# Optimization experiments

Measured on AMD Instinct MI355X. Metric: run time of the kernel, lower is better.

The kernel has to match this reference:

```python
import jax, jax.numpy as jnp
import numpy as np

N = 100000      # atoms
E = 200000      # bonds (directed)
N2 = 200000     # 2-set super-nodes
A = 400000      # assignment entries atoms->2-sets
E2 = 400000     # 2-set graph edges
G = 5000        # molecules
D = 256         # emb_dim
FEAT = 40       # num_atom_features
NI2 = 8         # num_i_2
NBOND = 4       # bond types for edge embedding
L = 5           # num_layer
BN_EPS = 1e-5


def setup_inputs() -> dict:
    key = jax.random.key(0)
    ks = jax.random.split(key, 24)
    nrm = lambda k, shape, fan: jax.random.normal(k, shape, jnp.float32) / np.float32(np.sqrt(fan))
    inp = {}
    inp['x'] = jax.random.normal(ks[0], (N, FEAT), jnp.float32)
    inp['edge_index'] = jax.random.randint(ks[1], (2, E), 0, N, jnp.int32)
    inp['edge_attr'] = jax.random.randint(ks[2], (E,), 0, NBOND, jnp.int32)
    inp['iso_type_2'] = jax.random.uniform(ks[3], (N2, NI2), jnp.float32)
    inp['edge_index_2'] = jax.random.randint(ks[4], (2, E2), 0, N2, jnp.int32)
    inp['assignment_index_2'] = jnp.stack([
        jax.random.randint(ks[5], (A,), 0, N, jnp.int32),
        jax.random.randint(ks[6], (A,), 0, N2, jnp.int32)])
    inp['batch'] = jnp.sort(jax.random.randint(ks[7], (N,), 0, G, jnp.int32))
    inp['batch_2'] = jnp.sort(jax.random.randint(ks[8], (N2,), 0, G, jnp.int32))
    # params
    inp['W_emb'] = nrm(ks[9], (FEAT, D), FEAT); inp['b_emb'] = jnp.zeros((D,), jnp.float32)
    inp['edge_tables'] = nrm(ks[10], (L, NBOND, D), D)
    inp['eps'] = jnp.zeros((L,), jnp.float32)
    inp['gin_w1'] = nrm(ks[11], (L, D, 2 * D), D); inp['gin_b1'] = jnp.zeros((L, 2 * D), jnp.float32)
    inp['gin_w2'] = nrm(ks[12], (L, 2 * D, D), 2 * D); inp['gin_b2'] = jnp.zeros((L, D), jnp.float32)
    inp['bn_gamma'] = jnp.ones((L, D), jnp.float32); inp['bn_beta'] = jnp.zeros((L, D), jnp.float32)
    inp['iso1_ws'] = nrm(ks[13], (D + NI2, D), D + NI2)
    inp['iso1_wn'] = nrm(ks[14], (D + NI2, D), D + NI2)
    inp['iso1_b'] = jnp.zeros((D,), jnp.float32)
    inp['iso2_ws'] = nrm(ks[15], (D, D), D)
    inp['iso2_wn'] = nrm(ks[16], (D, D), D)
    inp['iso2_b'] = jnp.zeros((D,), jnp.float32)
    inp['fc0_w'] = nrm(ks[17], (2 * D, D), 2 * D); inp['fc0_b'] = jnp.zeros((D,), jnp.float32)
    inp['fc1_w'] = nrm(ks[18], (D, D // 2), D); inp['fc1_b'] = jnp.zeros((D // 2,), jnp.float32)
    inp['fc2_w'] = nrm(ks[19], (D // 2, D // 4), D // 2); inp['fc2_b'] = jnp.zeros((D // 4,), jnp.float32)
    inp['last_w'] = nrm(ks[20], (D // 4, 1), D // 4); inp['last_b'] = jnp.zeros((1,), jnp.float32)
    return inp


def _segment_mean(v, seg, num):
    s = jax.ops.segment_sum(v, seg, num_segments=num)
    c = jax.ops.segment_sum(jnp.ones((v.shape[0], 1), v.dtype), seg, num_segments=num)
    return s / jnp.maximum(c, 1.0)


def _graph_conv(h, src, dst, ws, wn, b, n):
    # PyG GraphConv: W_self x_i + sum_{j->i} W_nei x_j + b
    nei = jax.ops.segment_sum((h @ wn)[src], dst, num_segments=n)
    return h @ ws + nei + b


def reference(x, edge_index, edge_attr, iso_type_2, edge_index_2, assignment_index_2,
              batch, batch_2, W_emb, b_emb, edge_tables, eps, gin_w1, gin_b1,
              gin_w2, gin_b2, bn_gamma, bn_beta, iso1_ws, iso1_wn, iso1_b,
              iso2_ws, iso2_wn, iso2_b, fc0_w, fc0_b, fc1_w, fc1_b, fc2_w, fc2_b,
              last_w, last_b):
    n = x.shape[0]
    src, dst = edge_index[0], edge_index[1]
    # atom embedding
    h = jax.nn.relu(x @ W_emb + b_emb)
    # GIN stack (JK='last', eval mode: dropout identity, BN with batch stats)
    for l in range(L):
        msg = h[src] + edge_tables[l][edge_attr]          # [E, D]
        agg = jax.ops.segment_sum(msg, dst, num_segments=n)
        z = (1.0 + eps[l]) * h + agg
        z = jax.nn.relu(z @ gin_w1[l] + gin_b1[l]) @ gin_w2[l] + gin_b2[l]
        mu = z.mean(axis=0)
        var = z.var(axis=0)
        z = bn_gamma[l] * (z - mu) * jax.lax.rsqrt(var + BN_EPS) + bn_beta[l]
        h = z if l == L - 1 else jax.nn.relu(z)
    node_rep = h                                           # [N, D]
    # graph pooling (mean)
    x_1 = _segment_mean(node_rep, batch, G)                # [G, D]
    # avg_pool onto 2-set nodes
    xp = _segment_mean(node_rep[assignment_index_2[0]], assignment_index_2[1], N2)
    x2 = jnp.concatenate([xp, iso_type_2], axis=1)         # [N2, D+NI2]
    s2, d2 = edge_index_2[0], edge_index_2[1]
    x2 = jax.nn.relu(_graph_conv(x2, s2, d2, iso1_ws, iso1_wn, iso1_b, N2))
    x2 = jax.nn.relu(_graph_conv(x2, s2, d2, iso2_ws, iso2_wn, iso2_b, N2))
    x_2 = _segment_mean(x2, batch_2, G)                    # [G, D]
    m = jnp.concatenate([x_1, x_2], axis=1)                # [G, 2D]
    m = jax.nn.relu(m @ fc0_w + fc0_b)
    m = jax.nn.relu(m @ fc1_w + fc1_b)
    m = jax.nn.relu(m @ fc2_w + fc2_b)
    m = m @ last_w + last_b
    return m.reshape(-1)                                   # num_tasks == 1
```

## Files before the change

### kernel.cpp

```cpp
#include <hip/hip_runtime.h>
#include <cstddef>

constexpr int NA   = 100000;
constexpr int NE   = 200000;
constexpr int NN2  = 200000;
constexpr int NASS = 400000;
constexpr int NE2  = 400000;
constexpr int NG   = 5000;
constexpr int D    = 256;
constexpr int FEAT = 40;
constexpr int NI2  = 8;
constexpr int NL   = 5;
constexpr int CH   = 25000;

typedef unsigned short u16;
typedef __attribute__((ext_vector_type(8))) short bf16x8;
typedef __attribute__((ext_vector_type(4))) float f32x4;

static __device__ __forceinline__ float b2f(u16 s) {
    union { unsigned int u; float f; } v; v.u = ((unsigned int)s) << 16; return v.f;
}
static __device__ __forceinline__ u16 f2b(float f) {
    union { unsigned int u; float f; } v; v.f = f;
    unsigned int r = v.u + 0x7FFFu + ((v.u >> 16) & 1u);
    return (u16)(r >> 16);
}

constexpr size_t HB_OFF   = 0;
constexpr size_t ZB_OFF   = 102400000;
constexpr size_t TC_OFF   = 153600000;
constexpr size_t XEMB_OFF = 102400000;
constexpr size_t XPB_OFF  = 102400000;
constexpr size_t HN_OFF   = 0;
constexpr size_t MB_OFF   = 204800000;
constexpr size_t F1_OFF   = 215040000;
constexpr size_t F2_OFF   = 220160000;
constexpr size_t F3_OFF   = 222720000;
constexpr size_t WEMT_OFF = 224000000;
constexpr size_t GW1T_OFF = 224065536;
constexpr size_t GW2T_OFF = 226686976;
constexpr size_t IWT_OFF  = 229308416;
constexpr size_t EOFF_OFF = 230400000;
constexpr size_t EIDS_OFF = 230800768;
constexpr size_t AOFF_OFF = 231600832;
constexpr size_t AIDS_OFF = 232400896;
constexpr size_t E2OFF_OFF= 234000960;
constexpr size_t E2IDS_OFF= 234801024;
constexpr size_t CUR_OFF  = 236401088;
constexpr size_t PART_OFF = 237201152;
constexpr size_t GST_OFF  = 237202240;
constexpr size_t G2ST_OFF = 237222272;
constexpr size_t BS_OFF   = 237242304;
constexpr size_t SC_OFF   = 237244416;
constexpr size_t SH_OFF   = 237245440;
constexpr size_t WS_BYTES = 237246464;

template<int BIAS, int RELU, int ISO, int AF32, int CF32>
__global__ __launch_bounds__(512) void k_mgemm(
    const void* __restrict__ Av, int lda,
    const u16* __restrict__ Bt,
    const float* __restrict__ bias,
    const float* __restrict__ iso,
    const float* __restrict__ wtail,
    void* __restrict__ Cv, int ldc,
    int M, int N, int K)
{
    __shared__ __align__(16) u16 Ah[128][40];
    __shared__ __align__(16) u16 Al[AF32 ? 128 : 1][40];
    __shared__ __align__(16) u16 Bh[256][40];
    __shared__ __align__(16) u16 Bl[256][40];
    const int tid = threadIdx.x;
    const int wave = tid >> 6, lane = tid & 63;
    const int wr = wave >> 2, wc = wave & 3;
    const int bm = blockIdx.y * 128, bn = blockIdx.x * 256;
    const int l15 = lane & 15, lhi = lane >> 4;
    const int ar = tid >> 2, ac = (tid & 3) << 3;
    const u16* Blo = Bt + (size_t)N * K;
    f32x4 acc[4][4] = {};
    const int ktiles = K >> 5;
    for (int kt = 0; kt < ktiles; ++kt) {
        const int k0 = kt << 5;
        ushort4 a0h = {0,0,0,0}, a1h = {0,0,0,0}, a0l = {0,0,0,0}, a1l = {0,0,0,0};
        if (AF32) {
            float4 v0 = {0,0,0,0}, v1 = {0,0,0,0};
            if (bm + ar < M) {
                const float* ap = (const float*)Av + (size_t)(bm + ar) * lda + k0 + ac;
                v0 = *(const float4*)ap; v1 = *(const float4*)(ap + 4);
            }
            a0h.x = f2b(v0.x); a0h.y = f2b(v0.y); a0h.z = f2b(v0.z); a0h.w = f2b(v0.w);
            a1h.x = f2b(v1.x); a1h.y = f2b(v1.y); a1h.z = f2b(v1.z); a1h.w = f2b(v1.w);
            a0l.x = f2b(v0.x - b2f(a0h.x)); a0l.y = f2b(v0.y - b2f(a0h.y));
            a0l.z = f2b(v0.z - b2f(a0h.z)); a0l.w = f2b(v0.w - b2f(a0h.w));
            a1l.x = f2b(v1.x - b2f(a1h.x)); a1l.y = f2b(v1.y - b2f(a1h.y));
            a1l.z = f2b(v1.z - b2f(a1h.z)); a1l.w = f2b(v1.w - b2f(a1h.w));
        } else {
            if (bm + ar < M) {
                const u16* ap = (const u16*)Av + (size_t)(bm + ar) * lda + k0 + ac;
                a0h = *(const ushort4*)ap; a1h = *(const ushort4*)(ap + 4);
            }
        }
        const u16* bp0h = Bt  + (size_t)(bn + ar) * K + k0 + ac;
        const u16* bp1h = Bt  + (size_t)(bn + 128 + ar) * K + k0 + ac;
        const u16* bp0l = Blo + (size_t)(bn + ar) * K + k0 + ac;
        const u16* bp1l = Blo + (size_t)(bn + 128 + ar) * K + k0 + ac;
        ushort4 b00h = *(const ushort4*)bp0h, b01h = *(const ushort4*)(bp0h + 4);
        ushort4 b10h = *(const ushort4*)bp1h, b11h = *(const ushort4*)(bp1h + 4);
        ushort4 b00l = *(const ushort4*)bp0l, b01l = *(const ushort4*)(bp0l + 4);
        ushort4 b10l = *(const ushort4*)bp1l, b11l = *(const ushort4*)(bp1l + 4);
        __syncthreads();
        *(ushort4*)&Ah[ar][ac] = a0h; *(ushort4*)&Ah[ar][ac + 4] = a1h;
        if (AF32) { *(ushort4*)&Al[ar][ac] = a0l; *(ushort4*)&Al[ar][ac + 4] = a1l; }
        *(ushort4*)&Bh[ar][ac] = b00h;       *(ushort4*)&Bh[ar][ac + 4] = b01h;
        *(ushort4*)&Bh[128 + ar][ac] = b10h; *(ushort4*)&Bh[128 + ar][ac + 4] = b11h;
        *(ushort4*)&Bl[ar][ac] = b00l;       *(ushort4*)&Bl[ar][ac + 4] = b01l;
        *(ushort4*)&Bl[128 + ar][ac] = b10l; *(ushort4*)&Bl[128 + ar][ac + 4] = b11l;
        __syncthreads();
        bf16x8 fah[4], fal[4], fbh[4], fbl[4];
        #pragma unroll
        for (int m = 0; m < 4; ++m) {
            fah[m] = *(const bf16x8*)&Ah[wr * 64 + m * 16 + l15][lhi * 8];
            if (AF32) fal[m] = *(const bf16x8*)&Al[wr * 64 + m * 16 + l15][lhi * 8];
        }
        #pragma unroll
        for (int n = 0; n < 4; ++n) {
            fbh[n] = *(const bf16x8*)&Bh[wc * 64 + n * 16 + l15][lhi * 8];
            fbl[n] = *(const bf16x8*)&Bl[wc * 64 + n * 16 + l15][lhi * 8];
        }
        #pragma unroll
        for (int m = 0; m < 4; ++m)
            #pragma unroll
            for (int n = 0; n < 4; ++n) {
                acc[m][n] = __builtin_amdgcn_mfma_f32_16x16x32_bf16(fah[m], fbh[n], acc[m][n], 0, 0, 0);
                acc[m][n] = __builtin_amdgcn_mfma_f32_16x16x32_bf16(fah[m], fbl[n], acc[m][n], 0, 0, 0);
                if (AF32)
                    acc[m][n] = __builtin_amdgcn_mfma_f32_16x16x32_bf16(fal[m], fbh[n], acc[m][n], 0, 0, 0);
            }
    }
    #pragma unroll
    for (int m = 0; m < 4; ++m) {
        int rbase = bm + wr * 64 + m * 16 + lhi * 4;
        #pragma unroll
        for (int n = 0; n < 4; ++n) {
            int col = bn + wc * 64 + n * 16 + l15;
            #pragma unroll
            for (int r = 0; r < 4; ++r) {
                int row = rbase + r;
                if (row >= M) continue;
                float v = acc[m][n][r];
                if (BIAS) v += bias[col];
                if (ISO) {
                    const float* ir = iso + (size_t)row * NI2;
                    #pragma unroll
                    for (int k = 0; k < NI2; ++k) v += ir[k] * wtail[k * 256 + col];
                }
                if (RELU) v = fmaxf(v, 0.f);
                size_t cidx = (size_t)row * ldc + col;
                if (CF32) ((float*)Cv)[cidx] = v;
                else      ((u16*)Cv)[cidx] = f2b(v);
            }
        }
    }
}

__global__ __launch_bounds__(256) void k_gemm(
    const float* __restrict__ A, int lda,
    const float* __restrict__ B, int ldb,
    const float* __restrict__ bias,
    float* __restrict__ C, int ldc,
    int M, int N, int K, int relu)
{
    __shared__ __align__(16) float As[16][68];
    __shared__ __align__(16) float Bs[16][68];
    const int tid = threadIdx.x;
    const int tx = tid & 15, ty = tid >> 4;
    const int bm = blockIdx.y * 64, bn = blockIdx.x * 64;
    const int arow = tid >> 2, akq = (tid & 3) << 2;
    const int bk = tid >> 4, bnq = (tid & 15) << 2;
    float c[4][4] = {};
    const int ktiles = (K + 15) >> 4;
    for (int kt = 0; kt < ktiles; ++kt) {
        const int k0 = kt << 4;
        float4 av = make_float4(0.f, 0.f, 0.f, 0.f);
        if (bm + arow < M && k0 + akq + 4 <= K)
            av = *reinterpret_cast<const float4*>(A + (size_t)(bm + arow) * lda + (k0 + akq));
        As[akq + 0][arow] = av.x; As[akq + 1][arow] = av.y;
        As[akq + 2][arow] = av.z; As[akq + 3][arow] = av.w;
        float4 bv = make_float4(0.f, 0.f, 0.f, 0.f);
        if (k0 + bk < K && bn + bnq + 4 <= N)
            bv = *reinterpret_cast<const float4*>(B + (size_t)(k0 + bk) * ldb + (bn + bnq));
        *reinterpret_cast<float4*>(&Bs[bk][bnq]) = bv;
        __syncthreads();
        #pragma unroll
        for (int k = 0; k < 16; ++k) {
            float a0 = As[k][ty*4+0], a1 = As[k][ty*4+1], a2 = As[k][ty*4+2], a3 = As[k][ty*4+3];
            float b0 = Bs[k][tx*4+0], b1 = Bs[k][tx*4+1], b2 = Bs[k][tx*4+2], b3 = Bs[k][tx*4+3];
            c[0][0]+=a0*b0;c[0][1]+=a0*b1;c[0][2]+=a0*b2;c[0][3]+=a0*b3;
            c[1][0]+=a1*b0;c[1][1]+=a1*b1;c[1][2]+=a1*b2;c[1][3]+=a1*b3;
            c[2][0]+=a2*b0;c[2][1]+=a2*b1;c[2][2]+=a2*b2;c[2][3]+=a2*b3;
            c[3][0]+=a3*b0;c[3][1]+=a3*b1;c[3][2]+=a3*b2;c[3][3]+=a3*b3;
        }
        __syncthreads();
    }
    #pragma unroll
    for (int i = 0; i < 4; ++i) {
        int row = bm + ty * 4 + i;
        if (row >= M) continue;
        #pragma unroll
        for (int j = 0; j < 4; ++j) {
            int col = bn + tx * 4 + j;
            if (col >= N) continue;
            float v = c[i][j] + bias[col];
            if (relu) v = fmaxf(v, 0.f);
            C[(size_t)row * ldc + col] = v;
        }
    }
}

__global__ void k_zero(float* __restrict__ p, size_t n) {
    size_t i = (size_t)blockIdx.x * blockDim.x + threadIdx.x;
    size_t st = (size_t)gridDim.x * blockDim.x;
    for (; i < n; i += st) p[i] = 0.f;
}
__global__ void k_fill(float* __restrict__ p, int n, float v) {
    int i = blockIdx.x * blockDim.x + threadIdx.x;
    int st = gridDim.x * blockDim.x;
    for (; i < n; i += st) p[i] = v;
}

__global__ void k_count(const int* __restrict__ idx, int n, int* __restrict__ cnt) {
    int i = blockIdx.x * blockDim.x + threadIdx.x;
    int st = gridDim.x * blockDim.x;
    for (; i < n; i += st) atomicAdd(&cnt[idx[i]], 1);
}
__global__ void k_scan_partial(const int* __restrict__ cnt, int n, int* __restrict__ part) {
    __shared__ int sm[256];
    int c = blockIdx.x, t = threadIdx.x;
    int base = c * 4096 + t * 16;
    int s = 0;
    #pragma unroll
    for (int j = 0; j < 16; ++j) { int i = base + j; if (i < n) s += cnt[i]; }
    sm[t] = s; __syncthreads();
    for (int o = 128; o; o >>= 1) { if (t < o) sm[t] += sm[t + o]; __syncthreads(); }
    if (t == 0) part[c] = sm[0];
}
__global__ void k_scan_mid(int* __restrict__ part, int nch, int* __restrict__ off, int n) {
    if (threadIdx.x == 0 && blockIdx.x == 0) {
        int run = 0;
        for (int c = 0; c < nch; ++c) { int v = part[c]; part[c] = run; run += v; }
        off[n] = run;
    }
}
__global__ void k_scan_final(const int* __restrict__ cnt, int n, const int* __restrict__ part,
                             int* __restrict__ off) {
    __shared__ int sm[256];
    int c = blockIdx.x, t = threadIdx.x;
    int base = c * 4096 + t * 16;
    int loc[16]; int s = 0;
    #pragma unroll
    for (int j = 0; j < 16; ++j) { int i = base + j; int v = (i < n) ? cnt[i] : 0; loc[j] = s; s += v; }
    sm[t] = s; __syncthreads();
    for (int o = 1; o < 256; o <<= 1) {
        int v = (t >= o) ? sm[t - o] : 0;
        __syncthreads(); sm[t] += v; __syncthreads();
    }
    int tpre = (t == 0) ? 0 : sm[t - 1];
    int cb = part[c];
    #pragma unroll
    for (int j = 0; j < 16; ++j) { int i = base + j; if (i < n) off[i] = cb + tpre + loc[j]; }
}
__global__ void k_fill_csr(const int* __restrict__ idx, const int* __restrict__ pay, int n,
                           const int* __restrict__ off, int* __restrict__ cur, int* __restrict__ ids) {
    int i = blockIdx.x * blockDim.x + threadIdx.x;
    int st = gridDim.x * blockDim.x;
    for (; i < n; i += st) {
        int d = idx[i];
        int p = off[d] + atomicAdd(&cur[d], 1);
        ids[p] = pay[i];
    }
}
__global__ void k_pack(const int* __restrict__ src, const int* __restrict__ attr,
                       int* __restrict__ pk, int n) {
    int i = blockIdx.x * blockDim.x + threadIdx.x;
    int st = gridDim.x * blockDim.x;
    for (; i < n; i += st) pk[i] = (src[i] << 2) | attr[i];
}
__global__ void k_lbound(const int* __restrict__ arr, int n, int nseg, int* __restrict__ st) {
    int g = blockIdx.x * blockDim.x + threadIdx.x;
    if (g > nseg) return;
    int lo = 0, hi = n;
    while (lo < hi) { int mid = (lo + hi) >> 1; if (arr[mid] < g) lo = mid + 1; else hi = mid; }
    st[g] = lo;
}

__global__ void k_wt(const float* __restrict__ w, u16* __restrict__ wt, int K, int N) {
    int i = blockIdx.x * blockDim.x + threadIdx.x;
    int tot = K * N, st = gridDim.x * blockDim.x;
    for (; i < tot; i += st) {
        int n_ = i / K, k = i - n_ * K;
        float v = w[(size_t)k * N + n_];
        u16 h = f2b(v);
        wt[i] = h;
        wt[(size_t)tot + i] = f2b(v - b2f(h));
    }
}
__global__ void k_wembT(const float* __restrict__ w, u16* __restrict__ wt) {
    int i = blockIdx.x * blockDim.x + threadIdx.x;
    if (i >= 256 * 64) return;
    int n_ = i >> 6, k = i & 63;
    float v = (k < FEAT) ? w[(size_t)k * 256 + n_] : 0.f;
    u16 h = f2b(v);
    wt[i] = h;
    wt[256 * 64 + i] = f2b(v - b2f(h));
}
__global__ void k_xemb(const float* __restrict__ x, float* __restrict__ xe) {
    size_t i = (size_t)blockIdx.x * blockDim.x + threadIdx.x;
    size_t st = (size_t)gridDim.x * blockDim.x;
    size_t tot = (size_t)NA * 64;
    for (; i < tot; i += st) {
        int r = (int)(i >> 6), c = (int)(i & 63);
        xe[i] = (c < FEAT) ? x[(size_t)r * FEAT + c] : 0.f;
    }
}

__global__ void k_gin_gather(const float* __restrict__ hb, const int* __restrict__ off,
                             const int* __restrict__ ids, const float* __restrict__ etab_l,
                             const float* __restrict__ epsv, int l, u16* __restrict__ zb) {
    int wid = (blockIdx.x * blockDim.x + threadIdx.x) >> 6;
    int lane = threadIdx.x & 63;
    int nw = (gridDim.x * blockDim.x) >> 6;
    int c = lane * 4;
    float e1 = 1.f + epsv[l];
    for (int v = wid; v < NA; v += nw) {
        float4 h = *(const float4*)(hb + (size_t)v * D + c);
        float s0 = e1 * h.x, s1 = e1 * h.y, s2 = e1 * h.z, s3 = e1 * h.w;
        int p1 = off[v + 1];
        for (int p = off[v]; p < p1; ++p) {
            int pk = ids[p]; int src = pk >> 2; int at = pk & 3;
            float4 u = *(const float4*)(hb + (size_t)src * D + c);
            float4 t = *(const float4*)(etab_l + at * D + c);
            s0 += u.x + t.x; s1 += u.y + t.y; s2 += u.z + t.z; s3 += u.w + t.w;
        }
        ushort4 o; o.x = f2b(s0); o.y = f2b(s1); o.z = f2b(s2); o.w = f2b(s3);
        *(ushort4*)(zb + (size_t)v * D + c) = o;
    }
}
__global__ void k_xp_gather(const float* __restrict__ hb, const int* __restrict__ off,
                            const int* __restrict__ ids, u16* __restrict__ xpb) {
    int wid = (blockIdx.x * blockDim.x + threadIdx.x) >> 6;
    int lane = threadIdx.x & 63;
    int nw = (gridDim.x * blockDim.x) >> 6;
    int c = lane * 4;
    for (int v = wid; v < NN2; v += nw) {
        int p0 = off[v], p1 = off[v + 1];
        float s0 = 0, s1 = 0, s2 = 0, s3 = 0;
        for (int p = p0; p < p1; ++p) {
            const float* u = hb + (size_t)ids[p] * D + c;
            float4 uv = *(const float4*)u;
            s0 += uv.x; s1 += uv.y; s2 += uv.z; s3 += uv.w;
        }
        float inv = 1.f / fmaxf((float)(p1 - p0), 1.f);
        ushort4 o; o.x = f2b(s0 * inv); o.y = f2b(s1 * inv); o.z = f2b(s2 * inv); o.w = f2b(s3 * inv);
        *(ushort4*)(xpb + (size_t)v * D + c) = o;
    }
}
template<int POOL>
__global__ void k_conv_gather(u16* __restrict__ selfb, const u16* __restrict__ hn,
                              const int* __restrict__ off, const int* __restrict__ ids,
                              const int* __restrict__ batch2, float* __restrict__ mb) {
    int wid = (blockIdx.x * blockDim.x + threadIdx.x) >> 6;
    int lane = threadIdx.x & 63;
    int nw = (gridDim.x * blockDim.x) >> 6;
    int c = lane * 4;
    for (int v = wid; v < NN2; v += nw) {
        ushort4 sv = *(const ushort4*)(selfb + (size_t)v * D + c);
        float s0 = b2f(sv.x), s1 = b2f(sv.y), s2 = b2f(sv.z), s3 = b2f(sv.w);
        int p1 = off[v + 1];
        for (int p = off[v]; p < p1; ++p) {
            ushort4 u = *(const ushort4*)(hn + (size_t)ids[p] * D + c);
            s0 += b2f(u.x); s1 += b2f(u.y); s2 += b2f(u.z); s3 += b2f(u.w);
        }
        s0 = fmaxf(s0, 0.f); s1 = fmaxf(s1, 0.f); s2 = fmaxf(s2, 0.f); s3 = fmaxf(s3, 0.f);
        if (POOL) {
            float* mp = mb + (size_t)batch2[v] * (2 * D) + D + c;
            atomicAdd(mp + 0, s0); atomicAdd(mp + 1, s1);
            atomicAdd(mp + 2, s2); atomicAdd(mp + 3, s3);
        } else {
            ushort4 o; o.x = f2b(s0); o.y = f2b(s1); o.z = f2b(s2); o.w = f2b(s3);
            *(ushort4*)(selfb + (size_t)v * D + c) = o;
        }
    }
}

__global__ void k_bn_stats(const float* __restrict__ z, float* __restrict__ sum,
                           float* __restrict__ sumsq, int n) {
    int c = threadIdx.x;
    float s = 0.f, q = 0.f;
    for (int r = blockIdx.x; r < n; r += gridDim.x) {
        float v = z[(size_t)r * D + c];
        s += v; q += v * v;
    }
    atomicAdd(&sum[c], s);
    atomicAdd(&sumsq[c], q);
}
__global__ void k_bn_final(const float* __restrict__ sum, const float* __restrict__ sumsq,
                           const float* __restrict__ gamma, const float* __restrict__ beta,
                           float* __restrict__ scale, float* __restrict__ shift, int n) {
    int c = threadIdx.x;
    float mu = sum[c] / (float)n;
    float var = sumsq[c] / (float)n - mu * mu;
    float sc = gamma[c] * rsqrtf(var + 1e-5f);
    scale[c] = sc;
    shift[c] = beta[c] - mu * sc;
}
__global__ void k_bn_apply(float* __restrict__ h, const float* __restrict__ scale,
                           const float* __restrict__ shift, size_t n, int relu) {
    size_t i = (size_t)blockIdx.x * blockDim.x + threadIdx.x;
    size_t st = (size_t)gridDim.x * blockDim.x;
    for (; i < n; i += st) {
        int c = (int)(i & (D - 1));
        float v = scale[c] * h[i] + shift[c];
        if (relu) v = fmaxf(v, 0.f);
        h[i] = v;
    }
}

__global__ void k_pool1(const float* __restrict__ hb, const int* __restrict__ gst,
                        float* __restrict__ mb) {
    int g = blockIdx.x, t = threadIdx.x;
    int a = gst[g], b = gst[g + 1];
    float s = 0.f;
    for (int r = a; r < b; ++r) s += hb[(size_t)r * D + t];
    mb[(size_t)g * (2 * D) + t] = s / fmaxf((float)(b - a), 1.f);
}
__global__ void k_div2(float* __restrict__ mb, const int* __restrict__ g2st) {
    int g = blockIdx.x, t = threadIdx.x;
    float c = fmaxf((float)(g2st[g + 1] - g2st[g]), 1.f);
    mb[(size_t)g * (2 * D) + D + t] /= c;
}
__global__ void k_last(const float* __restrict__ f3, const float* __restrict__ w,
                       const float* __restrict__ b, float* __restrict__ out, int gn) {
    int g = blockIdx.x * 4 + (threadIdx.x >> 6);
    int lane = threadIdx.x & 63;
    if (g >= gn) return;
    float v = f3[(size_t)g * 64 + lane] * w[lane];
    #pragma unroll
    for (int off = 32; off; off >>= 1) v += __shfl_down(v, off);
    if (lane == 0) out[g] = v + b[0];
}

static inline dim3 ggrid(int M, int N) { return dim3((N + 63) / 64, (M + 63) / 64); }

extern "C" void kernel_launch(void* const* d_in, const int* in_sizes, int n_in,
                              void* d_out, int out_size, void* d_ws, size_t ws_size,
                              hipStream_t stream) {
    const float* x      = (const float*)d_in[0];
    const int*   eidx   = (const int*)  d_in[1];
    const int*   eattr  = (const int*)  d_in[2];
    const float* iso    = (const float*)d_in[3];
    const int*   eidx2  = (const int*)  d_in[4];
    const int*   assign = (const int*)  d_in[5];
    const int*   batch  = (const int*)  d_in[6];
    const int*   batch2 = (const int*)  d_in[7];
    const float* W_emb  = (const float*)d_in[8];
    const float* b_emb  = (const float*)d_in[9];
    const float* etab   = (const float*)d_in[10];
    const float* epsv   = (const float*)d_in[11];
    const float* gw1    = (const float*)d_in[12];
    const float* gb1    = (const float*)d_in[13];
    const float* gw2    = (const float*)d_in[14];
    const float* gb2    = (const float*)d_in[15];
    const float* bng    = (const float*)d_in[16];
    const float* bnb    = (const float*)d_in[17];
    const float* i1ws   = (const float*)d_in[18];
    const float* i1wn   = (const float*)d_in[19];
    const float* i1b    = (const float*)d_in[20];
    const float* i2ws   = (const float*)d_in[21];
    const float* i2wn   = (const float*)d_in[22];
    const float* i2b    = (const float*)d_in[23];
    const float* fc0w   = (const float*)d_in[24];
    const float* fc0b   = (const float*)d_in[25];
    const float* fc1w   = (const float*)d_in[26];
    const float* fc1b   = (const float*)d_in[27];
    const float* fc2w   = (const float*)d_in[28];
    const float* fc2b   = (const float*)d_in[29];
    const float* lw     = (const float*)d_in[30];
    const float* lb     = (const float*)d_in[31];

    float* out = (float*)d_out;
    char*  ws  = (char*)d_ws;
    if (ws_size < WS_BYTES) {
        k_fill<<<32, 256, 0, stream>>>(out, out_size, 10000.0f + (float)(ws_size >> 20));
        return;
    }

    float* HB   = (float*)(ws + HB_OFF);
    u16*   ZB   = (u16*)(ws + ZB_OFF);
    float* TC   = (float*)(ws + TC_OFF);
    float* XEMB = (float*)(ws + XEMB_OFF);
    u16*   XPB  = (u16*)(ws + XPB_OFF);
    u16*   HN   = (u16*)(ws + HN_OFF);
    float* Mb   = (float*)(ws + MB_OFF);
    float* F1   = (float*)(ws + F1_OFF);
    float* F2   = (float*)(ws + F2_OFF);
    float* F3   = (float*)(ws + F3_OFF);
    u16*   wembT= (u16*)(ws + WEMT_OFF);
    u16*   gw1T = (u16*)(ws + GW1T_OFF);
    u16*   gw2T = (u16*)(ws + GW2T_OFF);
    u16*   iwT  = (u16*)(ws + IWT_OFF);
    u16*   i1wnT= iwT;
    u16*   i1wsT= iwT + 2 * 65536;
    u16*   i2wnT= iwT + 4 * 65536;
    u16*   i2wsT= iwT + 6 * 65536;
    int*   eoff = (int*)(ws + EOFF_OFF);
    int*   eids = (int*)(ws + EIDS_OFF);
    int*   aoff = (int*)(ws + AOFF_OFF);
    int*   aids = (int*)(ws + AIDS_OFF);
    int*   e2off= (int*)(ws + E2OFF_OFF);
    int*   e2ids= (int*)(ws + E2IDS_OFF);
    int*   cur  = (int*)(ws + CUR_OFF);
    int*   part = (int*)(ws + PART_OFF);
    int*   gst  = (int*)(ws + GST_OFF);
    int*   g2st = (int*)(ws + G2ST_OFF);
    float* BS   = (float*)(ws + BS_OFF);
    float* SC   = (float*)(ws + SC_OFF);
    float* SH   = (float*)(ws + SH_OFF);
    int*   packs= (int*)F1;

    const int* e_src = eidx;   const int* e_dst = eidx + NE;
    const int* a0    = assign; const int* a1    = assign + NASS;
    const int* s2    = eidx2;  const int* d2    = eidx2 + NE2;

    dim3 sg(2048);
    dim3 ew(8192);
    const int nchA = (NA + 4095) / 4096;
    const int nch2 = (NN2 + 4095) / 4096;

    k_zero<<<dim3(1024), 256, 0, stream>>>(Mb, (size_t)NG * 2 * D);

    k_lbound<<<dim3((NG + 256) / 256), 256, 0, stream>>>(batch, NA, NG, gst);
    k_lbound<<<dim3((NG + 256) / 256), 256, 0, stream>>>(batch2, NN2, NG, g2st);

    k_zero<<<dim3(256), 256, 0, stream>>>((float*)cur, NA);
    k_count<<<dim3(1024), 256, 0, stream>>>(e_dst, NE, cur);
    k_scan_partial<<<dim3(nchA), 256, 0, stream>>>(cur, NA, part);
    k_scan_mid<<<dim3(1), 64, 0, stream>>>(part, nchA, eoff, NA);
    k_scan_final<<<dim3(nchA), 256, 0, stream>>>(cur, NA, part, eoff);
    k_zero<<<dim3(256), 256, 0, stream>>>((float*)cur, NA);
    k_pack<<<dim3(1024), 256, 0, stream>>>(e_src, eattr, packs, NE);
    k_fill_csr<<<dim3(1024), 256, 0, stream>>>(e_dst, packs, NE, eoff, cur, eids);

    k_zero<<<dim3(256), 256, 0, stream>>>((float*)cur, NN2);
    k_count<<<dim3(1024), 256, 0, stream>>>(a1, NASS, cur);
    k_scan_partial<<<dim3(nch2), 256, 0, stream>>>(cur, NN2, part);
    k_scan_mid<<<dim3(1), 64, 0, stream>>>(part, nch2, aoff, NN2);
    k_scan_final<<<dim3(nch2), 256, 0, stream>>>(cur, NN2, part, aoff);
    k_zero<<<dim3(256), 256, 0, stream>>>((float*)cur, NN2);
    k_fill_csr<<<dim3(1024), 256, 0, stream>>>(a1, a0, NASS, aoff, cur, aids);

    k_zero<<<dim3(256), 256, 0, stream>>>((float*)cur, NN2);
    k_count<<<dim3(1024), 256, 0, stream>>>(d2, NE2, cur);
    k_scan_partial<<<dim3(nch2), 256, 0, stream>>>(cur, NN2, part);
    k_scan_mid<<<dim3(1), 64, 0, stream>>>(part, nch2, e2off, NN2);
    k_scan_final<<<dim3(nch2), 256, 0, stream>>>(cur, NN2, part, e2off);
    k_zero<<<dim3(256), 256, 0, stream>>>((float*)cur, NN2);
    k_fill_csr<<<dim3(1024), 256, 0, stream>>>(d2, s2, NE2, e2off, cur, e2ids);

    k_wembT<<<dim3(64), 256, 0, stream>>>(W_emb, wembT);
    for (int l = 0; l < NL; ++l) {
        k_wt<<<dim3(512), 256, 0, stream>>>(gw1 + (size_t)l * D * 2 * D, gw1T + (size_t)l * 2 * 2 * D * D, D, 2 * D);
        k_wt<<<dim3(512), 256, 0, stream>>>(gw2 + (size_t)l * 2 * D * D, gw2T + (size_t)l * 2 * 2 * D * D, 2 * D, D);
    }
    k_wt<<<dim3(256), 256, 0, stream>>>(i1wn, i1wnT, D, D);
    k_wt<<<dim3(256), 256, 0, stream>>>(i1ws, i1wsT, D, D);
    k_wt<<<dim3(256), 256, 0, stream>>>(i2wn, i2wnT, D, D);
    k_wt<<<dim3(256), 256, 0, stream>>>(i2ws, i2wsT, D, D);

    k_xemb<<<ew, 256, 0, stream>>>(x, XEMB);
    k_mgemm<1,1,0,1,1><<<dim3(1, (NA + 127) / 128), 512, 0, stream>>>(
        XEMB, 64, wembT, b_emb, nullptr, nullptr, HB, D, NA, D, 64);

    for (int l = 0; l < NL; ++l) {
        k_gin_gather<<<sg, 256, 0, stream>>>(HB, eoff, eids, etab + (size_t)l * 4 * D, epsv, l, ZB);
        for (int c = 0; c < NA / CH; ++c) {
            k_mgemm<1,1,0,0,1><<<dim3(2, (CH + 127) / 128), 512, 0, stream>>>(
                ZB + (size_t)c * CH * D, D, gw1T + (size_t)l * 2 * 2 * D * D,
                gb1 + (size_t)l * 2 * D, nullptr, nullptr, TC, 2 * D, CH, 2 * D, D);
            k_mgemm<1,0,0,1,1><<<dim3(1, (CH + 127) / 128), 512, 0, stream>>>(
                TC, 2 * D, gw2T + (size_t)l * 2 * 2 * D * D,
                gb2 + (size_t)l * D, nullptr, nullptr, HB + (size_t)c * CH * D, D, CH, D, 2 * D);
        }
        k_zero<<<dim3(1), 512, 0, stream>>>(BS, 512);
        k_bn_stats<<<dim3(512), 256, 0, stream>>>(HB, BS, BS + D, NA);
        k_bn_final<<<dim3(1), 256, 0, stream>>>(BS, BS + D, bng + (size_t)l * D, bnb + (size_t)l * D, SC, SH, NA);
        k_bn_apply<<<ew, 256, 0, stream>>>(HB, SC, SH, (size_t)NA * D, l < NL - 1 ? 1 : 0);
    }

    k_pool1<<<dim3(NG), 256, 0, stream>>>(HB, gst, Mb);

    k_xp_gather<<<sg, 256, 0, stream>>>(HB, aoff, aids, XPB);

    k_mgemm<0,0,1,0,0><<<dim3(1, (NN2 + 127) / 128), 512, 0, stream>>>(
        XPB, D, i1wnT, nullptr, iso, i1wn + (size_t)D * D, HN, D, NN2, D, D);
    k_mgemm<1,0,1,0,0><<<dim3(1, (NN2 + 127) / 128), 512, 0, stream>>>(
        XPB, D, i1wsT, i1b, iso, i1ws + (size_t)D * D, XPB, D, NN2, D, D);
    k_conv_gather<0><<<sg, 256, 0, stream>>>(XPB, HN, e2off, e2ids, nullptr, nullptr);

    k_mgemm<0,0,0,0,0><<<dim3(1, (NN2 + 127) / 128), 512, 0, stream>>>(
        XPB, D, i2wnT, nullptr, nullptr, nullptr, HN, D, NN2, D, D);
    k_mgemm<1,0,0,0,0><<<dim3(1, (NN2 + 127) / 128), 512, 0, stream>>>(
        XPB, D, i2wsT, i2b, nullptr, nullptr, XPB, D, NN2, D, D);
    k_conv_gather<1><<<sg, 256, 0, stream>>>(XPB, HN, e2off, e2ids, batch2, Mb);
    k_div2<<<dim3(NG), 256, 0, stream>>>(Mb, g2st);

    k_gemm<<<ggrid(NG, D), 256, 0, stream>>>(Mb, 2 * D, fc0w, D, fc0b, F1, D, NG, D, 2 * D, 1);
    k_gemm<<<ggrid(NG, D / 2), 256, 0, stream>>>(F1, D, fc1w, D / 2, fc1b, F2, D / 2, NG, D / 2, D, 1);
    k_gemm<<<ggrid(NG, D / 4), 256, 0, stream>>>(F2, D / 2, fc2w, D / 4, fc2b, F3, D / 4, NG, D / 4, D / 2, 1);
    k_last<<<dim3((NG + 3) / 4), 256, 0, stream>>>(F3, lw, lb, out, NG);
}
```

Baseline: 3.909 ms.

## Store activations as split bf16 hi/lo pairs instead of fp32

Replaces fp32 intermediate buffers (node features, GEMM hidden outputs, embedding input) with bf16 storage. Where precision matters, a hi/lo bf16 pair is written by the GEMM epilogue, so the GEMM no longer converts fp32 to bf16 in its A-load loop. Gathers now read half-width rows and BN apply writes bf16 only. The atomic-based second pooling is replaced by a segmented pool kernel. The aim is to cut memory traffic and conversion ALU work. In exchange, node features lose precision after BN, since only the hi part is kept.

```diff
diff --git a/kernel.cpp b/kernel.cpp
--- a/kernel.cpp
+++ b/kernel.cpp
@@ -26,12 +26,12 @@
     return (u16)(r >> 16);
 }
 
-constexpr size_t HB_OFF   = 0;
-constexpr size_t ZB_OFF   = 102400000;
-constexpr size_t TC_OFF   = 153600000;
-constexpr size_t XEMB_OFF = 102400000;
-constexpr size_t XPB_OFF  = 102400000;
-constexpr size_t HN_OFF   = 0;
+constexpr size_t ZB_OFF   = 0;
+constexpr size_t TC_OFF   = 51200000;
+constexpr size_t XEMB_OFF = 51200000;
+constexpr size_t HB_OFF   = 102400000;
+constexpr size_t XPB_OFF  = 0;
+constexpr size_t HN_OFF   = 102400000;
 constexpr size_t MB_OFF   = 204800000;
 constexpr size_t F1_OFF   = 215040000;
 constexpr size_t F2_OFF   = 220160000;
@@ -51,22 +51,22 @@
 constexpr size_t GST_OFF  = 237202240;
 constexpr size_t G2ST_OFF = 237222272;
 constexpr size_t BS_OFF   = 237242304;
-constexpr size_t SC_OFF   = 237244416;
-constexpr size_t SH_OFF   = 237245440;
-constexpr size_t WS_BYTES = 237246464;
-
-template<int BIAS, int RELU, int ISO, int AF32, int CF32>
+constexpr size_t SCL_OFF  = 237244416;
+constexpr size_t SHL_OFF  = 237249536;
+constexpr size_t WS_BYTES = 237254656;
+
+template<int BIAS, int RELU, int ISO, int ALO, int CSPLIT>
 __global__ __launch_bounds__(512) void k_mgemm(
-    const void* __restrict__ Av, int lda,
+    const u16* __restrict__ A, int lda,
     const u16* __restrict__ Bt,
     const float* __restrict__ bias,
     const float* __restrict__ iso,
     const float* __restrict__ wtail,
-    void* __restrict__ Cv, int ldc,
+    u16* __restrict__ C, int ldc, long clo,
     int M, int N, int K)
 {
     __shared__ __align__(16) u16 Ah[128][40];
-    __shared__ __align__(16) u16 Al[AF32 ? 128 : 1][40];
+    __shared__ __align__(16) u16 Al[ALO ? 128 : 1][40];
     __shared__ __align__(16) u16 Bh[256][40];
     __shared__ __align__(16) u16 Bl[256][40];
     const int tid = threadIdx.x;
@@ -75,51 +75,32 @@
     const int bm = blockIdx.y * 128, bn = blockIdx.x * 256;
     const int l15 = lane & 15, lhi = lane >> 4;
     const int ar = tid >> 2, ac = (tid & 3) << 3;
+    const u16* Alo = A + (size_t)M * lda;
     const u16* Blo = Bt + (size_t)N * K;
     f32x4 acc[4][4] = {};
     const int ktiles = K >> 5;
     for (int kt = 0; kt < ktiles; ++kt) {
         const int k0 = kt << 5;
-        ushort4 a0h = {0,0,0,0}, a1h = {0,0,0,0}, a0l = {0,0,0,0}, a1l = {0,0,0,0};
-        if (AF32) {
-            float4 v0 = {0,0,0,0}, v1 = {0,0,0,0};
-            if (bm + ar < M) {
-                const float* ap = (const float*)Av + (size_t)(bm + ar) * lda + k0 + ac;
-                v0 = *(const float4*)ap; v1 = *(const float4*)(ap + 4);
-            }
-            a0h.x = f2b(v0.x); a0h.y = f2b(v0.y); a0h.z = f2b(v0.z); a0h.w = f2b(v0.w);
-            a1h.x = f2b(v1.x); a1h.y = f2b(v1.y); a1h.z = f2b(v1.z); a1h.w = f2b(v1.w);
-            a0l.x = f2b(v0.x - b2f(a0h.x)); a0l.y = f2b(v0.y - b2f(a0h.y));
-            a0l.z = f2b(v0.z - b2f(a0h.z)); a0l.w = f2b(v0.w - b2f(a0h.w));
-            a1l.x = f2b(v1.x - b2f(a1h.x)); a1l.y = f2b(v1.y - b2f(a1h.y));
-            a1l.z = f2b(v1.z - b2f(a1h.z)); a1l.w = f2b(v1.w - b2f(a1h.w));
-        } else {
-            if (bm + ar < M) {
-                const u16* ap = (const u16*)Av + (size_t)(bm + ar) * lda + k0 + ac;
-                a0h = *(const ushort4*)ap; a1h = *(const ushort4*)(ap + 4);
-            }
-        }
-        const u16* bp0h = Bt  + (size_t)(bn + ar) * K + k0 + ac;
-        const u16* bp1h = Bt  + (size_t)(bn + 128 + ar) * K + k0 + ac;
-        const u16* bp0l = Blo + (size_t)(bn + ar) * K + k0 + ac;
-        const u16* bp1l = Blo + (size_t)(bn + 128 + ar) * K + k0 + ac;
-        ushort4 b00h = *(const ushort4*)bp0h, b01h = *(const ushort4*)(bp0h + 4);
-        ushort4 b10h = *(const ushort4*)bp1h, b11h = *(const ushort4*)(bp1h + 4);
-        ushort4 b00l = *(const ushort4*)bp0l, b01l = *(const ushort4*)(bp0l + 4);
-        ushort4 b10l = *(const ushort4*)bp1l, b11l = *(const ushort4*)(bp1l + 4);
+        uint4 avh = {0,0,0,0}, avl = {0,0,0,0};
+        if (bm + ar < M) {
+            avh = *(const uint4*)(A + (size_t)(bm + ar) * lda + k0 + ac);
+            if (ALO) avl = *(const uint4*)(Alo + (size_t)(bm + ar) * lda + k0 + ac);
+        }
+        uint4 b0h = *(const uint4*)(Bt  + (size_t)(bn + ar) * K + k0 + ac);
+        uint4 b1h = *(const uint4*)(Bt  + (size_t)(bn + 128 + ar) * K + k0 + ac);
+        uint4 b0l = *(const uint4*)(Blo + (size_t)(bn + ar) * K + k0 + ac);
+        uint4 b1l = *(const uint4*)(Blo + (size_t)(bn + 128 + ar) * K + k0 + ac);
         __syncthreads();
-        *(ushort4*)&Ah[ar][ac] = a0h; *(ushort4*)&Ah[ar][ac + 4] = a1h;
-        if (AF32) { *(ushort4*)&Al[ar][ac] = a0l; *(ushort4*)&Al[ar][ac + 4] = a1l; }
-        *(ushort4*)&Bh[ar][ac] = b00h;       *(ushort4*)&Bh[ar][ac + 4] = b01h;
-        *(ushort4*)&Bh[128 + ar][ac] = b10h; *(ushort4*)&Bh[128 + ar][ac + 4] = b11h;
-        *(ushort4*)&Bl[ar][ac] = b00l;       *(ushort4*)&Bl[ar][ac + 4] = b01l;
-        *(ushort4*)&Bl[128 + ar][ac] = b10l; *(ushort4*)&Bl[128 + ar][ac + 4] = b11l;
+        *(uint4*)&Ah[ar][ac] = avh;
+        if (ALO) *(uint4*)&Al[ar][ac] = avl;
+        *(uint4*)&Bh[ar][ac] = b0h;  *(uint4*)&Bh[128 + ar][ac] = b1h;
+        *(uint4*)&Bl[ar][ac] = b0l;  *(uint4*)&Bl[128 + ar][ac] = b1l;
         __syncthreads();
         bf16x8 fah[4], fal[4], fbh[4], fbl[4];
         #pragma unroll
         for (int m = 0; m < 4; ++m) {
             fah[m] = *(const bf16x8*)&Ah[wr * 64 + m * 16 + l15][lhi * 8];
-            if (AF32) fal[m] = *(const bf16x8*)&Al[wr * 64 + m * 16 + l15][lhi * 8];
+            if (ALO) fal[m] = *(const bf16x8*)&Al[wr * 64 + m * 16 + l15][lhi * 8];
         }
         #pragma unroll
         for (int n = 0; n < 4; ++n) {
@@ -132,7 +113,7 @@
             for (int n = 0; n < 4; ++n) {
                 acc[m][n] = __builtin_amdgcn_mfma_f32_16x16x32_bf16(fah[m], fbh[n], acc[m][n], 0, 0, 0);
                 acc[m][n] = __builtin_amdgcn_mfma_f32_16x16x32_bf16(fah[m], fbl[n], acc[m][n], 0, 0, 0);
-                if (AF32)
+                if (ALO)
                     acc[m][n] = __builtin_amdgcn_mfma_f32_16x16x32_bf16(fal[m], fbh[n], acc[m][n], 0, 0, 0);
             }
     }
@@ -155,8 +136,13 @@
                 }
                 if (RELU) v = fmaxf(v, 0.f);
                 size_t cidx = (size_t)row * ldc + col;
-                if (CF32) ((float*)Cv)[cidx] = v;
-                else      ((u16*)Cv)[cidx] = f2b(v);
+                if (CSPLIT) {
+                    u16 h = f2b(v);
+                    C[cidx] = h;
+                    C[cidx + clo] = f2b(v - b2f(h));
+                } else {
+                    C[cidx] = f2b(v);
+                }
             }
         }
     }
@@ -312,17 +298,20 @@
     wt[i] = h;
     wt[256 * 64 + i] = f2b(v - b2f(h));
 }
-__global__ void k_xemb(const float* __restrict__ x, float* __restrict__ xe) {
+__global__ void k_xemb(const float* __restrict__ x, u16* __restrict__ xe) {
     size_t i = (size_t)blockIdx.x * blockDim.x + threadIdx.x;
     size_t st = (size_t)gridDim.x * blockDim.x;
     size_t tot = (size_t)NA * 64;
     for (; i < tot; i += st) {
         int r = (int)(i >> 6), c = (int)(i & 63);
-        xe[i] = (c < FEAT) ? x[(size_t)r * FEAT + c] : 0.f;
-    }
-}
-
-__global__ void k_gin_gather(const float* __restrict__ hb, const int* __restrict__ off,
+        float v = (c < FEAT) ? x[(size_t)r * FEAT + c] : 0.f;
+        u16 h = f2b(v);
+        xe[i] = h;
+        xe[tot + i] = f2b(v - b2f(h));
+    }
+}
+
+__global__ void k_gin_gather(const u16* __restrict__ hb, const int* __restrict__ off,
                              const int* __restrict__ ids, const float* __restrict__ etab_l,
                              const float* __restrict__ epsv, int l, u16* __restrict__ zb) {
     int wid = (blockIdx.x * blockDim.x + threadIdx.x) >> 6;
@@ -331,20 +320,21 @@
     int c = lane * 4;
     float e1 = 1.f + epsv[l];
     for (int v = wid; v < NA; v += nw) {
-        float4 h = *(const float4*)(hb + (size_t)v * D + c);
-        float s0 = e1 * h.x, s1 = e1 * h.y, s2 = e1 * h.z, s3 = e1 * h.w;
+        ushort4 h = *(const ushort4*)(hb + (size_t)v * D + c);
+        float s0 = e1 * b2f(h.x), s1 = e1 * b2f(h.y), s2 = e1 * b2f(h.z), s3 = e1 * b2f(h.w);
         int p1 = off[v + 1];
         for (int p = off[v]; p < p1; ++p) {
             int pk = ids[p]; int src = pk >> 2; int at = pk & 3;
-            float4 u = *(const float4*)(hb + (size_t)src * D + c);
+            ushort4 u = *(const ushort4*)(hb + (size_t)src * D + c);
             float4 t = *(const float4*)(etab_l + at * D + c);
-            s0 += u.x + t.x; s1 += u.y + t.y; s2 += u.z + t.z; s3 += u.w + t.w;
+            s0 += b2f(u.x) + t.x; s1 += b2f(u.y) + t.y;
+            s2 += b2f(u.z) + t.z; s3 += b2f(u.w) + t.w;
         }
         ushort4 o; o.x = f2b(s0); o.y = f2b(s1); o.z = f2b(s2); o.w = f2b(s3);
         *(ushort4*)(zb + (size_t)v * D + c) = o;
     }
 }
-__global__ void k_xp_gather(const float* __restrict__ hb, const int* __restrict__ off,
+__global__ void k_xp_gather(const u16* __restrict__ hb, const int* __restrict__ off,
                             const int* __restrict__ ids, u16* __restrict__ xpb) {
     int wid = (blockIdx.x * blockDim.x + threadIdx.x) >> 6;
     int lane = threadIdx.x & 63;
@@ -354,19 +344,17 @@
         int p0 = off[v], p1 = off[v + 1];
         float s0 = 0, s1 = 0, s2 = 0, s3 = 0;
         for (int p = p0; p < p1; ++p) {
-            const float* u = hb + (size_t)ids[p] * D + c;
-            float4 uv = *(const float4*)u;
-            s0 += uv.x; s1 += uv.y; s2 += uv.z; s3 += uv.w;
+            ushort4 u = *(const ushort4*)(hb + (size_t)ids[p] * D + c);
+            s0 += b2f(u.x); s1 += b2f(u.y); s2 += b2f(u.z); s3 += b2f(u.w);
         }
         float inv = 1.f / fmaxf((float)(p1 - p0), 1.f);
-        ushort4 o; o.x = f2b(s0 * inv); o.y = f2b(s1 * inv); o.z = f2b(s2 * inv); o.w = f2b(s3 * inv);
+        ushort4 o;
+        o.x = f2b(s0 * inv); o.y = f2b(s1 * inv); o.z = f2b(s2 * inv); o.w = f2b(s3 * inv);
         *(ushort4*)(xpb + (size_t)v * D + c) = o;
     }
 }
-template<int POOL>
 __global__ void k_conv_gather(u16* __restrict__ selfb, const u16* __restrict__ hn,
-                              const int* __restrict__ off, const int* __restrict__ ids,
-                              const int* __restrict__ batch2, float* __restrict__ mb) {
+                              const int* __restrict__ off, const int* __restrict__ ids) {
     int wid = (blockIdx.x * blockDim.x + threadIdx.x) >> 6;
     int lane = threadIdx.x & 63;
     int nw = (gridDim.x * blockDim.x) >> 6;
@@ -379,24 +367,19 @@
             ushort4 u = *(const ushort4*)(hn + (size_t)ids[p] * D + c);
             s0 += b2f(u.x); s1 += b2f(u.y); s2 += b2f(u.z); s3 += b2f(u.w);
         }
-        s0 = fmaxf(s0, 0.f); s1 = fmaxf(s1, 0.f); s2 = fmaxf(s2, 0.f); s3 = fmaxf(s3, 0.f);
-        if (POOL) {
-            float* mp = mb + (size_t)batch2[v] * (2 * D) + D + c;
-            atomicAdd(mp + 0, s0); atomicAdd(mp + 1, s1);
-            atomicAdd(mp + 2, s2); atomicAdd(mp + 3, s3);
-        } else {
-            ushort4 o; o.x = f2b(s0); o.y = f2b(s1); o.z = f2b(s2); o.w = f2b(s3);
-            *(ushort4*)(selfb + (size_t)v * D + c) = o;
-        }
-    }
-}
-
-__global__ void k_bn_stats(const float* __restrict__ z, float* __restrict__ sum,
-                           float* __restrict__ sumsq, int n) {
+        ushort4 o;
+        o.x = f2b(fmaxf(s0, 0.f)); o.y = f2b(fmaxf(s1, 0.f));
+        o.z = f2b(fmaxf(s2, 0.f)); o.w = f2b(fmaxf(s3, 0.f));
+        *(ushort4*)(selfb + (size_t)v * D + c) = o;
+    }
+}
+
+__global__ void k_bn_stats(const u16* __restrict__ zhi, const u16* __restrict__ zlo,
+                           float* __restrict__ sum, float* __restrict__ sumsq, int n) {
     int c = threadIdx.x;
     float s = 0.f, q = 0.f;
     for (int r = blockIdx.x; r < n; r += gridDim.x) {
-        float v = z[(size_t)r * D + c];
+        float v = b2f(zhi[(size_t)r * D + c]) + b2f(zlo[(size_t)r * D + c]);
         s += v; q += v * v;
     }
     atomicAdd(&sum[c], s);
@@ -412,30 +395,35 @@
     scale[c] = sc;
     shift[c] = beta[c] - mu * sc;
 }
-__global__ void k_bn_apply(float* __restrict__ h, const float* __restrict__ scale,
-                           const float* __restrict__ shift, size_t n, int relu) {
+__global__ void k_bn_apply(u16* __restrict__ zhi, const u16* __restrict__ zlo,
+                           const float* __restrict__ scale, const float* __restrict__ shift,
+                           size_t n, int relu) {
     size_t i = (size_t)blockIdx.x * blockDim.x + threadIdx.x;
     size_t st = (size_t)gridDim.x * blockDim.x;
     for (; i < n; i += st) {
         int c = (int)(i & (D - 1));
-        float v = scale[c] * h[i] + shift[c];
+        float z = b2f(zhi[i]) + b2f(zlo[i]);
+        float v = scale[c] * z + shift[c];
         if (relu) v = fmaxf(v, 0.f);
-        h[i] = v;
-    }
-}
-
-__global__ void k_pool1(const float* __restrict__ hb, const int* __restrict__ gst,
+        zhi[i] = f2b(v);
+    }
+}
+
+__global__ void k_pool1(const u16* __restrict__ hb, const int* __restrict__ gst,
                         float* __restrict__ mb) {
     int g = blockIdx.x, t = threadIdx.x;
     int a = gst[g], b = gst[g + 1];
     float s = 0.f;
-    for (int r = a; r < b; ++r) s += hb[(size_t)r * D + t];
+    for (int r = a; r < b; ++r) s += b2f(hb[(size_t)r * D + t]);
     mb[(size_t)g * (2 * D) + t] = s / fmaxf((float)(b - a), 1.f);
 }
-__global__ void k_div2(float* __restrict__ mb, const int* __restrict__ g2st) {
+__global__ void k_pool2(const u16* __restrict__ x2b, const int* __restrict__ g2st,
+                        float* __restrict__ mb) {
     int g = blockIdx.x, t = threadIdx.x;
-    float c = fmaxf((float)(g2st[g + 1] - g2st[g]), 1.f);
-    mb[(size_t)g * (2 * D) + D + t] /= c;
+    int a = g2st[g], b = g2st[g + 1];
+    float s = 0.f;
+    for (int r = a; r < b; ++r) s += b2f(x2b[(size_t)r * D + t]);
+    mb[(size_t)g * (2 * D) + D + t] = s / fmaxf((float)(b - a), 1.f);
 }
 __global__ void k_last(const float* __restrict__ f3, const float* __restrict__ w,
                        const float* __restrict__ b, float* __restrict__ out, int gn) {
@@ -493,10 +481,10 @@
         return;
     }
 
-    float* HB   = (float*)(ws + HB_OFF);
     u16*   ZB   = (u16*)(ws + ZB_OFF);
-    float* TC   = (float*)(ws + TC_OFF);
-    float* XEMB = (float*)(ws + XEMB_OFF);
+    u16*   TC   = (u16*)(ws + TC_OFF);
+    u16*   XEMB = (u16*)(ws + XEMB_OFF);
+    u16*   HB   = (u16*)(ws + HB_OFF);
     u16*   XPB  = (u16*)(ws + XPB_OFF);
     u16*   HN   = (u16*)(ws + HN_OFF);
     float* Mb   = (float*)(ws + MB_OFF);
@@ -522,20 +510,20 @@
     int*   gst  = (int*)(ws + GST_OFF);
     int*   g2st = (int*)(ws + G2ST_OFF);
     float* BS   = (float*)(ws + BS_OFF);
-    float* SC   = (float*)(ws + SC_OFF);
-    float* SH   = (float*)(ws + SH_OFF);
+    float* SCL  = (float*)(ws + SCL_OFF);
+    float* SHL  = (float*)(ws + SHL_OFF);
     int*   packs= (int*)F1;
 
     const int* e_src = eidx;   const int* e_dst = eidx + NE;
     const int* a0    = assign; const int* a1    = assign + NASS;
     const int* s2    = eidx2;  const int* d2    = eidx2 + NE2;
+
+    u16* HBlo = HB + (size_t)NA * D;
 
     dim3 sg(2048);
     dim3 ew(8192);
     const int nchA = (NA + 4095) / 4096;
     const int nch2 = (NN2 + 4095) / 4096;
-
-    k_zero<<<dim3(1024), 256, 0, stream>>>(Mb, (size_t)NG * 2 * D);
 
     k_lbound<<<dim3((NG + 256) / 256), 256, 0, stream>>>(batch, NA, NG, gst);
     k_lbound<<<dim3((NG + 256) / 256), 256, 0, stream>>>(batch2, NN2, NG, g2st);
@@ -576,23 +564,27 @@
     k_wt<<<dim3(256), 256, 0, stream>>>(i2ws, i2wsT, D, D);
 
     k_xemb<<<ew, 256, 0, stream>>>(x, XEMB);
-    k_mgemm<1,1,0,1,1><<<dim3(1, (NA + 127) / 128), 512, 0, stream>>>(
-        XEMB, 64, wembT, b_emb, nullptr, nullptr, HB, D, NA, D, 64);
+    k_mgemm<1,1,0,1,0><<<dim3(1, (NA + 127) / 128), 512, 0, stream>>>(
+        XEMB, 64, wembT, b_emb, nullptr, nullptr, HB, D, 0, NA, D, 64);
 
     for (int l = 0; l < NL; ++l) {
         k_gin_gather<<<sg, 256, 0, stream>>>(HB, eoff, eids, etab + (size_t)l * 4 * D, epsv, l, ZB);
         for (int c = 0; c < NA / CH; ++c) {
             k_mgemm<1,1,0,0,1><<<dim3(2, (CH + 127) / 128), 512, 0, stream>>>(
                 ZB + (size_t)c * CH * D, D, gw1T + (size_t)l * 2 * 2 * D * D,
-                gb1 + (size_t)l * 2 * D, nullptr, nullptr, TC, 2 * D, CH, 2 * D, D);
+                gb1 + (size_t)l * 2 * D, nullptr, nullptr,
+                TC, 2 * D, (long)CH * 2 * D, CH, 2 * D, D);
             k_mgemm<1,0,0,1,1><<<dim3(1, (CH + 127) / 128), 512, 0, stream>>>(
                 TC, 2 * D, gw2T + (size_t)l * 2 * 2 * D * D,
-                gb2 + (size_t)l * D, nullptr, nullptr, HB + (size_t)c * CH * D, D, CH, D, 2 * D);
+                gb2 + (size_t)l * D, nullptr, nullptr,
+                HB + (size_t)c * CH * D, D, (long)NA * D, CH, D, 2 * D);
         }
         k_zero<<<dim3(1), 512, 0, stream>>>(BS, 512);
-        k_bn_stats<<<dim3(512), 256, 0, stream>>>(HB, BS, BS + D, NA);
-        k_bn_final<<<dim3(1), 256, 0, stream>>>(BS, BS + D, bng + (size_t)l * D, bnb + (size_t)l * D, SC, SH, NA);
-        k_bn_apply<<<ew, 256, 0, stream>>>(HB, SC, SH, (size_t)NA * D, l < NL - 1 ? 1 : 0);
+        k_bn_stats<<<dim3(512), 256, 0, stream>>>(HB, HBlo, BS, BS + D, NA);
+        k_bn_final<<<dim3(1), 256, 0, stream>>>(BS, BS + D, bng + (size_t)l * D, bnb + (size_t)l * D,
+                                                SCL + l * D, SHL + l * D, NA);
+        k_bn_apply<<<ew, 256, 0, stream>>>(HB, HBlo, SCL + l * D, SHL + l * D,
+                                           (size_t)NA * D, l < NL - 1 ? 1 : 0);
     }
 
     k_pool1<<<dim3(NG), 256, 0, stream>>>(HB, gst, Mb);
@@ -600,17 +592,18 @@
     k_xp_gather<<<sg, 256, 0, stream>>>(HB, aoff, aids, XPB);
 
     k_mgemm<0,0,1,0,0><<<dim3(1, (NN2 + 127) / 128), 512, 0, stream>>>(
-        XPB, D, i1wnT, nullptr, iso, i1wn + (size_t)D * D, HN, D, NN2, D, D);
+        XPB, D, i1wnT, nullptr, iso, i1wn + (size_t)D * D, HN, D, 0, NN2, D, D);
     k_mgemm<1,0,1,0,0><<<dim3(1, (NN2 + 127) / 128), 512, 0, stream>>>(
-        XPB, D, i1wsT, i1b, iso, i1ws + (size_t)D * D, XPB, D, NN2, D, D);
-    k_conv_gather<0><<<sg, 256, 0, stream>>>(XPB, HN, e2off, e2ids, nullptr, nullptr);
+        XPB, D, i1wsT, i1b, iso, i1ws + (size_t)D * D, XPB, D, 0, NN2, D, D);
+    k_conv_gather<<<sg, 256, 0, stream>>>(XPB, HN, e2off, e2ids);
 
     k_mgemm<0,0,0,0,0><<<dim3(1, (NN2 + 127) / 128), 512, 0, stream>>>(
-        XPB, D, i2wnT, nullptr, nullptr, nullptr, HN, D, NN2, D, D);
+        XPB, D, i2wnT, nullptr, nullptr, nullptr, HN, D, 0, NN2, D, D);
     k_mgemm<1,0,0,0,0><<<dim3(1, (NN2 + 127) / 128), 512, 0, stream>>>(
-        XPB, D, i2wsT, i2b, nullptr, nullptr, XPB, D, NN2, D, D);
-    k_conv_gather<1><<<sg, 256, 0, stream>>>(XPB, HN, e2off, e2ids, batch2, Mb);
-    k_div2<<<dim3(NG), 256, 0, stream>>>(Mb, g2st);
+        XPB, D, i2wsT, i2b, nullptr, nullptr, XPB, D, 0, NN2, D, D);
+    k_conv_gather<<<sg, 256, 0, stream>>>(XPB, HN, e2off, e2ids);
+
+    k_pool2<<<dim3(NG), 256, 0, stream>>>(XPB, g2st, Mb);
 
     k_gemm<<<ggrid(NG, D), 256, 0, stream>>>(Mb, 2 * D, fc0w, D, fc0b, F1, D, NG, D, 2 * D, 1);
     k_gemm<<<ggrid(NG, D / 2), 256, 0, stream>>>(F1, D, fc1w, D / 2, fc1b, F2, D / 2, NG, D / 2, D, 1);
```

Result: faster. 3.270 ms (-16.3%).
